# Kernel optimization log

Hardware: AMD Instinct MI355X
Metric: run time of the kernel (lower is better)

The kernel has to match this reference:

```python
import jax, jax.numpy as jnp
import numpy as np

BSZ = 4
SL = 4096
NPAD = 8192  # next power of two >= 2*SL (preconvolve)
K = 16       # num_eigh
D = 128      # n_embd
KU = 3       # k_u
NM = 2       # num_models (residual boosting)
NL = 2       # n_layers per SpectralSSM
DIN = 64     # vocab / d_in
DOUT = 64    # d_out
HID = 512    # scale * n_embd
EPS = 1e-6


def _top_eigh(sl, k):
    # Hankel matrix Z[i,j] = 2 / ((i+j)^3 - (i+j)), 1-indexed
    idx = np.arange(1, sl + 1, dtype=np.float64)
    s = idx[:, None] + idx[None, :]
    Z = 2.0 / (s ** 3 - s)
    w, v = np.linalg.eigh(Z)
    return np.abs(w[-k:]).astype(np.float32), v[:, -k:].astype(np.float32)


def setup_inputs() -> dict:
    key = jax.random.key(0)
    ks = jax.random.split(key, 12)
    sigma_np, phi_np = _top_eigh(SL, K)
    mx = DOUT ** (-0.5)
    std = 0.02
    return {
        "inputs": jax.random.randint(ks[0], (BSZ, SL), 0, DIN),
        "targets": jax.random.randint(ks[1], (BSZ, SL), 0, DOUT),
        "sigma": jnp.asarray(sigma_np),
        "phi": jnp.asarray(phi_np),
        "embed_w": std * jax.random.normal(ks[2], (NM, DIN, D), jnp.float32),
        "rn_w": jnp.ones((NM, NL, D), jnp.float32),
        "M_u": jax.random.uniform(ks[3], (NM, NL, KU, D, D), jnp.float32, -mx, mx),
        "M_phi_plus": std * jax.random.normal(ks[4], (NM, NL, K, D, D), jnp.float32),
        "M_phi_minus": std * jax.random.normal(ks[5], (NM, NL, K, D, D), jnp.float32),
        "fc1_w": std * jax.random.normal(ks[6], (NM, NL, 2 * HID, D), jnp.float32),
        "fc2_w": std * jax.random.normal(ks[7], (NM, NL, D, HID), jnp.float32),
        "out_w": std * jax.random.normal(ks[8], (NM, DOUT, D), jnp.float32),
    }


def _rms(x, w):
    return x * jax.lax.rsqrt(jnp.mean(x * x, axis=-1, keepdims=True) + EPS) * w


def _mlp(x, w1, w2):
    h = x @ w1.T                      # (b, s, 2*HID)
    y, gate = h[..., :HID], h[..., HID:]
    return (y * jax.nn.silu(gate)) @ w2.T


def _stu(x, V, alt, Mp, Mm, Mu):
    # spectral FFT long convolution with K eigenfilters
    U = jnp.fft.rfft(x, n=NPAD, axis=1)                                   # (b, F, d)
    Up = jnp.fft.irfft(V[None, :, :, None] * U[:, :, None, :], n=NPAD, axis=1)[:, :SL]  # (b, s, K, d)
    Ua = jnp.fft.rfft(x * alt[None, :, None], n=NPAD, axis=1)
    Um = jnp.fft.irfft(V[None, :, :, None] * Ua[:, :, None, :], n=NPAD, axis=1)[:, :SL]
    y = jnp.einsum('bski,kio->bso', Up, Mp) + jnp.einsum('bski,kio->bso', Um, Mm)
    ar = jnp.einsum('bsd,do->bso', x, Mu[0])
    for i in range(1, KU):
        xs = jnp.pad(x, ((0, 0), (i, 0), (0, 0)))[:, :SL]
        ar = ar + jnp.einsum('bsd,do->bso', xs, Mu[i])
    return y + ar


def reference(inputs, targets, sigma, phi, embed_w, rn_w, M_u, M_phi_plus,
              M_phi_minus, fc1_w, fc2_w, out_w):
    phi_s = phi * sigma[None, :] ** 0.25                 # fold sigma^{1/4} into filters
    V = jnp.fft.rfft(phi_s, n=NPAD, axis=0)              # (F, K), preconvolve
    alt = ((-1.0) ** jnp.arange(SL)).astype(phi.dtype)

    residual = jax.nn.one_hot(targets, DOUT, dtype=phi.dtype)
    total = None
    for m in range(NM):
        x = embed_w[m][inputs]                           # (b, s, d)
        for l in range(NL):
            z = x
            x = x + _stu(_rms(x, rn_w[m, l]), V, alt,
                         M_phi_plus[m, l], M_phi_minus[m, l], M_u[m, l])
            x = x + _mlp(x, fc1_w[m, l], fc2_w[m, l])
            x = x + z
        logits = x @ out_w[m].T                          # (b, s, DOUT)
        total = logits if total is None else total + logits
        residual = residual - jax.lax.stop_gradient(logits)  # boosting target for next model
    return total
```

## Files before the change

### kernel.cpp

```cpp
#include <hip/hip_runtime.h>
#include <hip/hip_bf16.h>
#include <cstdint>

typedef unsigned short u16;
typedef __attribute__((ext_vector_type(8))) short bf16x8;
typedef __attribute__((ext_vector_type(4))) float f32x4;

#define N_ROWS 16384

__device__ __forceinline__ float bf2f(u16 u){ union{unsigned i; float f;} v; v.i = ((unsigned)u)<<16; return v.f; }
__device__ __forceinline__ u16 f2bf(float f){ union{float f; unsigned i;} v; v.f = f; unsigned r = v.i + 0x7fffu + ((v.i>>16)&1u); return (u16)(r>>16); }

__device__ __forceinline__ void gl2lds(const u16* g, u16* l){
  __builtin_amdgcn_global_load_lds((const __attribute__((address_space(1))) void*)g,
                                   (__attribute__((address_space(3))) void*)l, 16, 0, 0);
}


__global__ __launch_bounds__(256) void buildT_k(const float* __restrict__ phi, const float* __restrict__ sigma,
                                                u16* __restrict__ T){
  int idx = blockIdx.x*256 + threadIdx.x;
  int t2 = idx & 63;
  int tt = (idx>>6) & 127;
  int o  = (idx>>13) & 31;
  int k  = idx>>18;
  float sp = powf(sigma[k], 0.25f);
  int d0 = o*128 + tt - t2*2;
  float v0 = (d0   >= 0) ? phi[(size_t)d0*16 + k]*sp     : 0.f;
  float v1 = (d0-1 >= 0) ? phi[(size_t)(d0-1)*16 + k]*sp : 0.f;
  ushort2 u; u.x = f2bf(v0); u.y = f2bf(v1);
  ((ushort2*)T)[idx] = u;
}

__global__ __launch_bounds__(256) void castw_k(const float* __restrict__ Mp, const float* __restrict__ Mm,
                                               u16* __restrict__ W){
  int z = blockIdx.z; int ml = z>>5, k = (z>>1)&15, pm = z&1;
  const float* src = (pm ? Mm : Mp) + (size_t)(ml*16 + k)*16384;
  u16* dst = W + (size_t)ml*(2048*256) + (size_t)(k*128)*256 + pm*128;
  __shared__ float t[32][33];
  int ty = threadIdx.x>>5, tx = threadIdx.x&31;
  int i0 = blockIdx.x*32, o0 = blockIdx.y*32;
#pragma unroll
  for (int j=0;j<4;++j) t[ty+j*8][tx] = src[(size_t)(i0+ty+j*8)*128 + o0+tx];
  __syncthreads();
#pragma unroll
  for (int j=0;j<4;++j){
    int o = o0 + ty + j*8, i = i0 + tx;
    dst[(size_t)o*256 + i] = f2bf(t[tx][ty+j*8]);
  }
}

__global__ __launch_bounds__(256) void castmu_k(const float* __restrict__ Mu, u16* __restrict__ MuT){
  int z = blockIdx.z; int ml = z/3, j = z%3;
  const float* src = Mu + (size_t)(ml*3 + j)*16384;
  u16* dst = MuT + (size_t)ml*(128*384) + j*128;
  __shared__ float t[32][33];
  int ty = threadIdx.x>>5, tx = threadIdx.x&31;
  int i0 = blockIdx.x*32, o0 = blockIdx.y*32;
#pragma unroll
  for (int jj=0;jj<4;++jj) t[ty+jj*8][tx] = src[(size_t)(i0+ty+jj*8)*128 + o0+tx];
  __syncthreads();
#pragma unroll
  for (int jj=0;jj<4;++jj){
    int o = o0 + ty + jj*8, i = i0 + tx;
    dst[(size_t)o*384 + i] = f2bf(t[tx][ty+jj*8]);
  }
}

__global__ __launch_bounds__(256) void castf_k(const float* __restrict__ src, u16* __restrict__ dst, int n4){
  int i = blockIdx.x*256 + threadIdx.x;
  if (i < n4){
    float4 v = ((const float4*)src)[i];
    ushort4 u; u.x=f2bf(v.x); u.y=f2bf(v.y); u.z=f2bf(v.z); u.w=f2bf(v.w);
    ((ushort4*)dst)[i] = u;
  }
}


__global__ __launch_bounds__(256) void embed_k(const int* __restrict__ tok, const float* __restrict__ E,
                                               float* __restrict__ x){
  int idx = blockIdx.x*256 + threadIdx.x;
  int r = idx>>5, q = idx&31;
  int t = tok[r];
  ((float4*)(x + (size_t)r*128))[q] = ((const float4*)(E + (size_t)t*128))[q];
}

__global__ __launch_bounds__(256) void rms_k(const float* __restrict__ x, const float* __restrict__ w,
                                             u16* __restrict__ Xcat, u16* __restrict__ Xar){
  int wave = threadIdx.x>>6, lane = threadIdx.x&63;
  int r = blockIdx.x*4 + wave;
  float2 xv = ((const float2*)(x + (size_t)r*128))[lane];
  float ss = xv.x*xv.x + xv.y*xv.y;
  for (int off=32; off; off>>=1) ss += __shfl_xor(ss, off, 64);
  float sc = rsqrtf(ss*(1.f/128.f) + 1e-6f);
  float2 wv = ((const float2*)w)[lane];
  float a = xv.x*sc*wv.x, b = xv.y*sc*wv.y;
  int s = r & 4095;
  float sg = (s & 1) ? -1.f : 1.f;
  ushort2* row = (ushort2*)(Xcat + (size_t)r*256);
  ushort2 u0; u0.x = f2bf(a);    u0.y = f2bf(b);
  ushort2 u1; u1.x = f2bf(a*sg); u1.y = f2bf(b*sg);
  row[lane]      = u0;
  row[64 + lane] = u1;
  ushort2 z2; z2.x = 0; z2.y = 0;
#pragma unroll
  for (int j=0;j<3;++j){
    if (s + j < 4096) ((ushort2*)(Xar + (size_t)(r+j)*384 + j*128))[lane] = u0;
    if (s < j)        ((ushort2*)(Xar + (size_t)r*384     + j*128))[lane] = z2;
  }
}

__global__ __launch_bounds__(256) void mid_k(const float* __restrict__ x, const float* __restrict__ Y,
                                             const u16* __restrict__ Yp, float* __restrict__ xmid,
                                             u16* __restrict__ xmbf){
  size_t idx = (size_t)blockIdx.x*256 + threadIdx.x;
  float4 xv = ((const float4*)x)[idx];
  float4 a  = ((const float4*)Y)[idx];
  const size_t P = (size_t)N_ROWS*32;
#pragma unroll
  for (int g=0; g<16; ++g){
    ushort4 v = ((const ushort4*)Yp)[idx + (size_t)g*P];
    a.x += bf2f(v.x); a.y += bf2f(v.y); a.z += bf2f(v.z); a.w += bf2f(v.w);
  }
  float4 r; r.x = xv.x+a.x; r.y = xv.y+a.y; r.z = xv.z+a.z; r.w = xv.w+a.w;
  ((float4*)xmid)[idx] = r;
  ushort4 u; u.x=f2bf(r.x); u.y=f2bf(r.y); u.z=f2bf(r.z); u.w=f2bf(r.w);
  ((ushort4*)xmbf)[idx] = u;
}

__global__ __launch_bounds__(256) void logits_k(const float* __restrict__ x, const u16* __restrict__ Wt,
                                                float* __restrict__ out, int accum){
  __shared__ u16 lw[64*130];
  for (int i = threadIdx.x; i < 8192; i += 256) lw[(i>>7)*130 + (i&127)] = Wt[i];
  __syncthreads();
  int wave = threadIdx.x>>6, lane = threadIdx.x&63;
  int r = blockIdx.x*4 + wave;
  const float* xr = x + (size_t)r*128;
  float acc = 0.f;
#pragma unroll
  for (int i=0;i<128;i+=4){
    float4 xv = *(const float4*)&xr[i];
    acc += xv.x*bf2f(lw[lane*130+i  ]) + xv.y*bf2f(lw[lane*130+i+1])
         + xv.z*bf2f(lw[lane*130+i+2]) + xv.w*bf2f(lw[lane*130+i+3]);
  }
  size_t o = (size_t)r*64 + lane;
  out[o] = accum ? (out[o] + acc) : acc;
}

template<int EPI>
__global__ __launch_bounds__(256) void gemm_k(const u16* __restrict__ A, int lda,
    const u16* __restrict__ Bt, int ldb, int Kdim, int ldc,
    u16* __restrict__ obf, float* __restrict__ of32,
    const float* __restrict__ e1, float* __restrict__ e2)
{
  __shared__ u16 Al[128*64];
  __shared__ u16 Bl[128*64];
  const int tid = threadIdx.x, w = tid>>6, lane = tid&63;
  const int wr = w>>1, wc = w&1;
  const int r0 = blockIdx.x*128, c0 = blockIdx.y*128;
  const int ccs = (((lane&7) ^ (lane>>3)))*8;
  f32x4 acc[4][4] = {};
  for (int k0 = 0; k0 < Kdim; k0 += 64){
#pragma unroll
    for (int i=0;i<4;++i){
      const int rr = w*32 + i*8 + (lane>>3);
      gl2lds(A  + (size_t)(r0+rr)*lda + k0 + ccs, &Al[(w*32+i*8)*64]);
      gl2lds(Bt + (size_t)(c0+rr)*ldb + k0 + ccs, &Bl[(w*32+i*8)*64]);
    }
    __syncthreads();
#pragma unroll
    for (int ks=0; ks<2; ++ks){
      const int rc = (((ks*4 + (lane>>4)) ^ (lane&7)))*8;
      bf16x8 av[4], bv[4];
#pragma unroll
      for (int mi=0;mi<4;++mi) av[mi] = *(const bf16x8*)&Al[(wr*64+mi*16+(lane&15))*64 + rc];
#pragma unroll
      for (int ni=0;ni<4;++ni) bv[ni] = *(const bf16x8*)&Bl[(wc*64+ni*16+(lane&15))*64 + rc];
#pragma unroll
      for (int mi=0;mi<4;++mi)
#pragma unroll
        for (int ni=0;ni<4;++ni)
          acc[mi][ni] = __builtin_amdgcn_mfma_f32_16x16x32_bf16(av[mi], bv[ni], acc[mi][ni], 0,0,0);
    }
    __syncthreads();
  }
  const int lr = (lane>>4)*4, lc = lane&15;
#pragma unroll
  for (int mi=0;mi<4;++mi){
#pragma unroll
    for (int ni=0;ni<4;++ni){
      const int gr = r0 + wr*64 + mi*16 + lr;
      const int gc = c0 + wc*64 + ni*16 + lc;
      if (EPI == 1){
#pragma unroll
        for (int j=0;j<4;++j) obf[(size_t)(gr+j)*ldc + gc] = f2bf(acc[mi][ni][j]);
      }
    }
  }
}

template<int EPI>
__global__ __launch_bounds__(256) void gemm64_k(const u16* __restrict__ A, int lda,
    const u16* __restrict__ Bt, int ldb, int Kdim, int ldc,
    float* __restrict__ of32, const float* __restrict__ e1, float* __restrict__ e2)
{
  __shared__ u16 Al[64*64];
  __shared__ u16 Bl[128*64];
  const int tid = threadIdx.x, w = tid>>6, lane = tid&63;
  const int r0 = blockIdx.x*64;
  const int l8 = lane>>3;
  const int ccs = (((lane&7) ^ l8))*8;
  f32x4 acc[4][2] = {};
  for (int k0 = 0; k0 < Kdim; k0 += 64){
#pragma unroll
    for (int i=0;i<2;++i){
      const int rr = w*16 + i*8 + l8;
      gl2lds(A + (size_t)(r0+rr)*lda + k0 + ccs, &Al[(w*16+i*8)*64]);
    }
#pragma unroll
    for (int i=0;i<4;++i){
      const int rr = w*32 + i*8 + l8;
      gl2lds(Bt + (size_t)rr*ldb + k0 + ccs, &Bl[(w*32+i*8)*64]);
    }
    __syncthreads();
#pragma unroll
    for (int ks=0; ks<2; ++ks){
      const int rc = (((ks*4 + (lane>>4)) ^ (lane&7)))*8;
      bf16x8 av[4], bv[2];
#pragma unroll
      for (int mi=0;mi<4;++mi) av[mi] = *(const bf16x8*)&Al[(mi*16+(lane&15))*64 + rc];
#pragma unroll
      for (int ni=0;ni<2;++ni) bv[ni] = *(const bf16x8*)&Bl[(w*32+ni*16+(lane&15))*64 + rc];
#pragma unroll
      for (int mi=0;mi<4;++mi)
#pragma unroll
        for (int ni=0;ni<2;++ni)
          acc[mi][ni] = __builtin_amdgcn_mfma_f32_16x16x32_bf16(av[mi], bv[ni], acc[mi][ni], 0,0,0);
    }
    __syncthreads();
  }
  const int lr = (lane>>4)*4, lc = lane&15;
#pragma unroll
  for (int mi=0;mi<4;++mi){
#pragma unroll
    for (int ni=0;ni<2;++ni){
      const int gr = r0 + mi*16 + lr;
      const int gc = w*32 + ni*16 + lc;
      if (EPI == 0){
#pragma unroll
        for (int j=0;j<4;++j) of32[(size_t)(gr+j)*ldc + gc] = acc[mi][ni][j];
      } else {
#pragma unroll
        for (int j=0;j<4;++j){ const size_t id = (size_t)(gr+j)*ldc + gc; e2[id] = acc[mi][ni][j] + e1[id] + e2[id]; }
      }
    }
  }
}

__global__ __launch_bounds__(256) void gemmgate_k(const u16* __restrict__ A,
    const u16* __restrict__ f1T, u16* __restrict__ hg)
{
  __shared__ u16 Al[128*64];
  __shared__ u16 Bl[128*64];
  __shared__ u16 sg[128*68];
  const int tid = threadIdx.x, w = tid>>6, lane = tid&63;
  const int wr = w>>1, wc = w&1;
  const int r0 = blockIdx.x*128, gj = blockIdx.y;
  const int ccs = (((lane&7) ^ (lane>>3)))*8;
  f32x4 acc[4][4] = {};
  for (int k0 = 0; k0 < 128; k0 += 64){
#pragma unroll
    for (int i=0;i<4;++i){
      const int rr = w*32 + i*8 + (lane>>3);
      const int br = (rr < 64) ? (gj*64 + rr) : (512 + gj*64 + rr - 64);
      gl2lds(A   + (size_t)(r0+rr)*128 + k0 + ccs, &Al[(w*32+i*8)*64]);
      gl2lds(f1T + (size_t)br*128     + k0 + ccs, &Bl[(w*32+i*8)*64]);
    }
    __syncthreads();
#pragma unroll
    for (int ks=0; ks<2; ++ks){
      const int rc = (((ks*4 + (lane>>4)) ^ (lane&7)))*8;
      bf16x8 av[4], bv[4];
#pragma unroll
      for (int mi=0;mi<4;++mi) av[mi] = *(const bf16x8*)&Al[(wr*64+mi*16+(lane&15))*64 + rc];
#pragma unroll
      for (int ni=0;ni<4;++ni) bv[ni] = *(const bf16x8*)&Bl[(wc*64+ni*16+(lane&15))*64 + rc];
#pragma unroll
      for (int mi=0;mi<4;++mi)
#pragma unroll
        for (int ni=0;ni<4;++ni)
          acc[mi][ni] = __builtin_amdgcn_mfma_f32_16x16x32_bf16(av[mi], bv[ni], acc[mi][ni], 0,0,0);
    }
    __syncthreads();
  }
  const int lr = (lane>>4)*4, lc = lane&15;
  if (wc == 1){
#pragma unroll
    for (int mi=0;mi<4;++mi)
#pragma unroll
      for (int ni=0;ni<4;++ni){
        const int rl = wr*64 + mi*16 + lr;
        const int cl = ni*16 + lc;
#pragma unroll
        for (int j=0;j<4;++j){
          float g = acc[mi][ni][j];
          sg[(size_t)(rl+j)*68 + cl] = f2bf(g/(1.f+expf(-g)));
        }
      }
  }
  __syncthreads();
  if (wc == 0){
#pragma unroll
    for (int mi=0;mi<4;++mi)
#pragma unroll
      for (int ni=0;ni<4;++ni){
        const int rl = wr*64 + mi*16 + lr;
        const int cl = ni*16 + lc;
#pragma unroll
        for (int j=0;j<4;++j){
          float g = bf2f(sg[(size_t)(rl+j)*68 + cl]);
          hg[(size_t)(r0+rl+j)*512 + gj*64 + cl] = f2bf(acc[mi][ni][j]*g);
        }
      }
  }
}

__global__ __launch_bounds__(256) void timemix_k(const u16* __restrict__ T, const u16* __restrict__ G,
                                                 u16* __restrict__ Yp)
{
  __shared__ u16 Al[128*64];
  __shared__ u16 Bl[128*64];
  const int bid = blockIdx.x;
  const int k  = bid & 15;
  const int b  = (bid>>4) & 3;
  const int qq = bid>>6;
  const int tid = threadIdx.x, w = tid>>6, lane = tid&63;
  const int wr = w>>1, wc = w&1;
  const int ccs = (((lane&7) ^ (lane>>3)))*8;
  const u16* Tk = T + (size_t)k*32*16384;
  const u16* Gk = G + (size_t)(k*128)*16384 + b*4096;
  u16* o = Yp + (size_t)k*((size_t)N_ROWS*128) + (size_t)b*4096*128;
  const int lr = (lane>>4)*4, lc = lane&15;
  for (int qi = 0; qi < 2; ++qi){
    const int q = qi ? (31-qq) : qq;
    f32x4 acc[4][4] = {};
    for (int p = 0; p <= q; ++p){
      const u16* Ab = Tk + (size_t)(q-p)*16384;
      const u16* Bb = Gk + (size_t)p*128;
#pragma unroll
      for (int hh=0; hh<2; ++hh){
        const int k0 = hh*64;
#pragma unroll
        for (int i=0;i<4;++i){
          const int rr = w*32 + i*8 + (lane>>3);
          gl2lds(Ab + (size_t)rr*128   + k0 + ccs, &Al[(w*32+i*8)*64]);
          gl2lds(Bb + (size_t)rr*16384 + k0 + ccs, &Bl[(w*32+i*8)*64]);
        }
        __syncthreads();
#pragma unroll
        for (int ks=0; ks<2; ++ks){
          const int rc = (((ks*4 + (lane>>4)) ^ (lane&7)))*8;
          bf16x8 av[4], bv[4];
#pragma unroll
          for (int mi=0;mi<4;++mi) av[mi] = *(const bf16x8*)&Al[(wr*64+mi*16+(lane&15))*64 + rc];
#pragma unroll
          for (int ni=0;ni<4;++ni) bv[ni] = *(const bf16x8*)&Bl[(wc*64+ni*16+(lane&15))*64 + rc];
#pragma unroll
          for (int mi=0;mi<4;++mi)
#pragma unroll
            for (int ni=0;ni<4;++ni)
              acc[mi][ni] = __builtin_amdgcn_mfma_f32_16x16x32_bf16(av[mi], bv[ni], acc[mi][ni], 0,0,0);
        }
        __syncthreads();
      }
    }
#pragma unroll
    for (int mi=0;mi<4;++mi){
#pragma unroll
      for (int ni=0;ni<4;++ni){
        const int grl = q*128 + wr*64 + mi*16 + lr;
        const int gc  = wc*64 + ni*16 + lc;
#pragma unroll
        for (int j=0;j<4;++j) o[(size_t)(grl + j)*128 + gc] = f2bf(acc[mi][ni][j]);
      }
    }
  }
}

extern "C" void kernel_launch(void* const* d_in, const int* in_sizes, int n_in,
                              void* d_out, int out_size, void* d_ws, size_t ws_size,
                              hipStream_t stream)
{
  const int*   inputs = (const int*)d_in[0];
  const float* sigma  = (const float*)d_in[2];
  const float* phi    = (const float*)d_in[3];
  const float* embed  = (const float*)d_in[4];
  const float* rnw    = (const float*)d_in[5];
  const float* Mu     = (const float*)d_in[6];
  const float* Mp     = (const float*)d_in[7];
  const float* Mm     = (const float*)d_in[8];
  const float* fc1    = (const float*)d_in[9];
  const float* fc2    = (const float*)d_in[10];
  const float* outw   = (const float*)d_in[11];
  float* out = (float*)d_out;
  char* ws = (char*)d_ws;
  size_t off = 0;
  auto alloc = [&](size_t bytes){ size_t o = off; off += (bytes + 255) & ~(size_t)255; return o; };
  u16*   T    = (u16*)  (ws + alloc((size_t)16*32*16384*2));
  u16*   Wcat = (u16*)  (ws + alloc((size_t)4*2048*256*2));
  u16*   MuT  = (u16*)  (ws + alloc((size_t)4*128*384*2));
  u16*   f1T  = (u16*)  (ws + alloc((size_t)524288*2));
  u16*   f2T  = (u16*)  (ws + alloc((size_t)262144*2));
  u16*   owT  = (u16*)  (ws + alloc((size_t)16384*2));
  float* x    = (float*)(ws + alloc((size_t)N_ROWS*128*4));
  float* Y    = (float*)(ws + alloc((size_t)N_ROWS*128*4));
  u16*   Ypb  = (u16*)  (ws + alloc((size_t)16*N_ROWS*128*2));
  float* xmid = (float*)(ws + alloc((size_t)N_ROWS*128*4));
  u16*   xmbf = (u16*)  (ws + alloc((size_t)N_ROWS*128*2));
  u16*   big  = (u16*)  (ws + alloc((size_t)2048*16384*2));
  u16*   Xar  = Ypb;
  u16*   Xcat = Ypb + (size_t)N_ROWS*384;
  u16*   Gt = big;
  u16*   hg = big;

  buildT_k <<<16384, 256, 0, stream>>>(phi, sigma, T);
  castw_k  <<<dim3(4,4,128), 256, 0, stream>>>(Mp, Mm, Wcat);
  castmu_k <<<dim3(4,4,12),  256, 0, stream>>>(Mu, MuT);
  castf_k  <<<512, 256, 0, stream>>>(fc1,  f1T, 131072);
  castf_k  <<<256, 256, 0, stream>>>(fc2,  f2T, 65536);
  castf_k  <<<16,  256, 0, stream>>>(outw, owT, 4096);

  for (int m = 0; m < 2; ++m){
    embed_k<<<2048, 256, 0, stream>>>(inputs, embed + (size_t)m*8192, x);
    for (int l = 0; l < 2; ++l){
      const int ml = m*2 + l;
      rms_k<<<4096, 256, 0, stream>>>(x, rnw + ml*128, Xcat, Xar);
      gemm64_k<0><<<dim3(256,1), 256, 0, stream>>>(Xar, 384, MuT + (size_t)ml*128*384, 384, 384, 128,
                                                   Y, nullptr, nullptr);
      gemm_k<1><<<dim3(16,128), 256, 0, stream>>>(Wcat + (size_t)ml*2048*256, 256, Xcat, 256, 256, 16384,
                                                  Gt, nullptr, nullptr, nullptr);
      timemix_k<<<1024, 256, 0, stream>>>(T, Gt, Ypb);
      mid_k<<<2048, 256, 0, stream>>>(x, Y, Ypb, xmid, xmbf);
      gemmgate_k<<<dim3(128,8), 256, 0, stream>>>(xmbf, f1T + (size_t)ml*1024*128, hg);
      gemm64_k<3><<<dim3(256,1), 256, 0, stream>>>(hg, 512, f2T + (size_t)ml*128*512, 512, 512, 128,
                                                   nullptr, xmid, x);
    }
    logits_k<<<4096, 256, 0, stream>>>(x, owT + (size_t)m*8192, out, m);
  }
}
```

Measured before the change: 1.108 ms.

## Rewrite timemix kernel with 512-thread blocks, wider N tile, and triple-buffered LDS pipeline

The time-mixing Toeplitz GEMM kernel now uses 8 waves per block and computes a 128x256 output tile that covers two batch elements at once, so each loaded T tile is reused across both. Global-to-LDS loads are triple-buffered and prefetched two steps ahead, with partial vmcnt waits and s_setprio around the MFMA bursts so that loads overlap compute instead of being serialised by a full barrier. This halves the block count and uses more LDS per block (occupancy of one block per CU), which could leave the GPU underfilled given the causal triangular load imbalance.

```diff
diff --git a/kernel.cpp b/kernel.cpp
--- a/kernel.cpp
+++ b/kernel.cpp
@@ -325,63 +325,100 @@
   }
 }
 
-__global__ __launch_bounds__(256) void timemix_k(const u16* __restrict__ T, const u16* __restrict__ G,
-                                                 u16* __restrict__ Yp)
+__global__ __launch_bounds__(512, 1) void timemix8_k(const u16* __restrict__ T, const u16* __restrict__ G,
+                                                     u16* __restrict__ Yp)
 {
-  __shared__ u16 Al[128*64];
-  __shared__ u16 Bl[128*64];
+  __shared__ u16 lds[3][24576];
   const int bid = blockIdx.x;
   const int k  = bid & 15;
-  const int b  = (bid>>4) & 3;
-  const int qq = bid>>6;
+  const int bp = (bid>>4) & 1;
+  const int qp = bid>>5;
   const int tid = threadIdx.x, w = tid>>6, lane = tid&63;
-  const int wr = w>>1, wc = w&1;
-  const int ccs = (((lane&7) ^ (lane>>3)))*8;
+  const int wr = w>>2, wc = w&3;
+  const int fr = lane&15;
+  const int l8 = lane>>3;
+  const int swz = ((lane&7) ^ l8)*8;
+  const int rbase = w*8 + l8;
   const u16* Tk = T + (size_t)k*32*16384;
-  const u16* Gk = G + (size_t)(k*128)*16384 + b*4096;
-  u16* o = Yp + (size_t)k*((size_t)N_ROWS*128) + (size_t)b*4096*128;
-  const int lr = (lane>>4)*4, lc = lane&15;
-  for (int qi = 0; qi < 2; ++qi){
-    const int q = qi ? (31-qq) : qq;
+  const u16* Gq = G + (size_t)(k*128)*16384 + (size_t)(bp*2)*4096;
+  u16* oY = Yp + (size_t)k*((size_t)N_ROWS*128) + (size_t)(bp*2)*4096*128;
+
+  for (int sp = 0; sp < 2; ++sp){
+    const int q = sp ? (31-qp) : qp;
+    const int TT = 2*(q+1);
+
+    auto stageA = [&](int ts, int buf, int r){
+      const int p = ts>>1, h = ts&1;
+      gl2lds(Tk + (size_t)(q-p)*16384 + (size_t)(r*64 + rbase)*128 + h*64 + swz,
+             &lds[buf][(r*64 + w*8)*64]);
+    };
+    auto stageB = [&](int ts, int buf, int bi, int r){
+      const int p = ts>>1, h = ts&1;
+      gl2lds(Gq + (size_t)(r*64 + rbase)*16384 + (size_t)bi*4096 + (size_t)p*128 + h*64 + swz,
+             &lds[buf][8192 + bi*8192 + (r*64 + w*8)*64]);
+    };
+
+    stageA(0,0,0); stageA(0,0,1); stageB(0,0,0,0); stageB(0,0,0,1); stageB(0,0,1,0); stageB(0,0,1,1);
+    stageA(1,1,0); stageA(1,1,1); stageB(1,1,0,0); stageB(1,1,0,1); stageB(1,1,1,0); stageB(1,1,1,1);
+    asm volatile("s_waitcnt vmcnt(6)" ::: "memory");
+    __builtin_amdgcn_s_barrier();
+
     f32x4 acc[4][4] = {};
-    for (int p = 0; p <= q; ++p){
-      const u16* Ab = Tk + (size_t)(q-p)*16384;
-      const u16* Bb = Gk + (size_t)p*128;
-#pragma unroll
-      for (int hh=0; hh<2; ++hh){
-        const int k0 = hh*64;
-#pragma unroll
-        for (int i=0;i<4;++i){
-          const int rr = w*32 + i*8 + (lane>>3);
-          gl2lds(Ab + (size_t)rr*128   + k0 + ccs, &Al[(w*32+i*8)*64]);
-          gl2lds(Bb + (size_t)rr*16384 + k0 + ccs, &Bl[(w*32+i*8)*64]);
-        }
-        __syncthreads();
-#pragma unroll
-        for (int ks=0; ks<2; ++ks){
-          const int rc = (((ks*4 + (lane>>4)) ^ (lane&7)))*8;
-          bf16x8 av[4], bv[4];
-#pragma unroll
-          for (int mi=0;mi<4;++mi) av[mi] = *(const bf16x8*)&Al[(wr*64+mi*16+(lane&15))*64 + rc];
-#pragma unroll
-          for (int ni=0;ni<4;++ni) bv[ni] = *(const bf16x8*)&Bl[(wc*64+ni*16+(lane&15))*64 + rc];
-#pragma unroll
-          for (int mi=0;mi<4;++mi)
-#pragma unroll
-            for (int ni=0;ni<4;++ni)
-              acc[mi][ni] = __builtin_amdgcn_mfma_f32_16x16x32_bf16(av[mi], bv[ni], acc[mi][ni], 0,0,0);
-        }
-        __syncthreads();
-      }
-    }
+    int cur = 0;
+    for (int t = 0; t < TT; ++t){
+      const int sb = (cur+2 >= 3) ? cur-1 : cur+2;
+      const bool st = (t+2 < TT);
+      {
+        const int rc = (((lane>>4)) ^ (fr&7))*8;
+        bf16x8 av[4], bv[4];
+#pragma unroll
+        for (int mi=0;mi<4;++mi) av[mi] = *(const bf16x8*)&lds[cur][(wr*64+mi*16+fr)*64 + rc];
+#pragma unroll
+        for (int ni=0;ni<4;++ni) bv[ni] = *(const bf16x8*)&lds[cur][8192 + (wc>>1)*8192 + ((wc&1)*64+ni*16+fr)*64 + rc];
+        if (st){ stageA(t+2,sb,0); stageA(t+2,sb,1); stageB(t+2,sb,0,0); }
+        __builtin_amdgcn_s_barrier();
+        __builtin_amdgcn_s_setprio(1);
+#pragma unroll
+        for (int mi=0;mi<4;++mi)
+#pragma unroll
+          for (int ni=0;ni<4;++ni)
+            acc[mi][ni] = __builtin_amdgcn_mfma_f32_16x16x32_bf16(av[mi], bv[ni], acc[mi][ni], 0,0,0);
+        __builtin_amdgcn_s_setprio(0);
+        __builtin_amdgcn_s_barrier();
+      }
+      {
+        const int rc = ((4 + (lane>>4)) ^ (fr&7))*8;
+        bf16x8 av[4], bv[4];
+#pragma unroll
+        for (int mi=0;mi<4;++mi) av[mi] = *(const bf16x8*)&lds[cur][(wr*64+mi*16+fr)*64 + rc];
+#pragma unroll
+        for (int ni=0;ni<4;++ni) bv[ni] = *(const bf16x8*)&lds[cur][8192 + (wc>>1)*8192 + ((wc&1)*64+ni*16+fr)*64 + rc];
+        if (st){ stageB(t+2,sb,0,1); stageB(t+2,sb,1,0); stageB(t+2,sb,1,1); }
+        __builtin_amdgcn_s_barrier();
+        __builtin_amdgcn_s_setprio(1);
+#pragma unroll
+        for (int mi=0;mi<4;++mi)
+#pragma unroll
+          for (int ni=0;ni<4;++ni)
+            acc[mi][ni] = __builtin_amdgcn_mfma_f32_16x16x32_bf16(av[mi], bv[ni], acc[mi][ni], 0,0,0);
+        __builtin_amdgcn_s_setprio(0);
+        if (st) asm volatile("s_waitcnt vmcnt(6)" ::: "memory");
+        else    asm volatile("s_waitcnt vmcnt(0)" ::: "memory");
+        __builtin_amdgcn_s_barrier();
+      }
+      cur = (cur==2) ? 0 : cur+1;
+    }
+    const int lr = (lane>>4)*4, lc = lane&15;
 #pragma unroll
     for (int mi=0;mi<4;++mi){
 #pragma unroll
       for (int ni=0;ni<4;++ni){
-        const int grl = q*128 + wr*64 + mi*16 + lr;
-        const int gc  = wc*64 + ni*16 + lc;
-#pragma unroll
-        for (int j=0;j<4;++j) o[(size_t)(grl + j)*128 + gc] = f2bf(acc[mi][ni][j]);
+        const int tg = q*128 + wr*64 + mi*16 + lr;
+        const int n  = wc*64 + ni*16 + lc;
+        const int bi = n>>7, o = n&127;
+#pragma unroll
+        for (int jj=0;jj<4;++jj)
+          oY[((size_t)bi*4096 + tg + jj)*(size_t)128 + o] = f2bf(acc[mi][ni][jj]);
       }
     }
   }
@@ -439,7 +476,7 @@
                                                    Y, nullptr, nullptr);
       gemm_k<1><<<dim3(16,128), 256, 0, stream>>>(Wcat + (size_t)ml*2048*256, 256, Xcat, 256, 256, 16384,
                                                   Gt, nullptr, nullptr, nullptr);
-      timemix_k<<<1024, 256, 0, stream>>>(T, Gt, Ypb);
+      timemix8_k<<<512, 512, 0, stream>>>(T, Gt, Ypb);
       mid_k<<<2048, 256, 0, stream>>>(x, Y, Ypb, xmid, xmbf);
       gemmgate_k<<<dim3(128,8), 256, 0, stream>>>(xmbf, f1T + (size_t)ml*1024*128, hg);
       gemm64_k<3><<<dim3(256,1), 256, 0, stream>>>(hg, 512, f2T + (size_t)ml*128*512, 512, 512, 128,
```

Result: no change. 1.117 ms (+0.8%).
